# Optimization experiments

Hardware: AMD Instinct MI355X
Metric: run time of the kernel (lower is better)

The kernel has to match this reference:

```python
import jax, jax.numpy as jnp
import numpy as np

# Norse-style LIF constants (LIFParameters defaults, method='super', alpha=100)
DT = 0.001
TAU_SYN_INV = 200.0
TAU_MEM_INV = 100.0
V_TH = 1.0
V_LEAK = 0.0
V_RESET = 0.0
ALPHA = 100.0

@jax.custom_vjp
def heaviside(x):
    return (x > 0).astype(x.dtype)

def _heaviside_fwd(x):
    return heaviside(x), x

def _heaviside_bwd(x, g):
    # SuperSpike surrogate: 1 / (alpha*|x| + 1)^2
    return (g / (ALPHA * jnp.abs(x) + 1.0) ** 2,)

heaviside.defvjp(_heaviside_fwd, _heaviside_bwd)

def lif_step(v, i, inp_cur):
    # explicit-Euler LIF: membrane decays toward leak driven by synaptic current,
    # synaptic current decays, spikes reset membrane, input arrives as current jump
    v_dec = v + DT * TAU_MEM_INV * ((V_LEAK - v) + i)
    i_dec = i * (1.0 - DT * TAU_SYN_INV)
    z = heaviside(v_dec - V_TH)
    v_new = (1.0 - z) * v_dec + z * V_RESET
    i_new = i_dec + inp_cur
    return z, v_new, i_new

def li_step(v, i, inp_cur):
    # leaky integrator (non-spiking readout)
    v_new = v + DT * TAU_MEM_INV * ((V_LEAK - v) + i)
    i_new = i * (1.0 - DT * TAU_SYN_INV) + inp_cur
    return v_new, i_new


def setup_inputs() -> dict:
    key = jax.random.key(0)
    k1, k2, k3 = jax.random.split(key, 3)
    T, B = 64, 128
    FS2, H1, HC, OC, OUT = 4096, 2048, 2, 4, 10
    spl1, spl2 = FS2 // HC, H1 // OC
    x = jax.random.uniform(k1, (T, B, FS2), dtype=jnp.float32)
    w_hidden = jax.random.normal(k2, (HC, spl1, H1), dtype=jnp.float32) / np.sqrt(spl1)
    w_out = jax.random.normal(k3, (OC, spl2, OUT), dtype=jnp.float32) / np.sqrt(spl2)
    return {"x": x, "w_hidden": w_hidden, "w_out": w_out}


def reference(x, w_hidden, w_out):
    T, B, FS2 = x.shape
    HC, SPL1, H1 = w_hidden.shape
    OC, SPL2, OUT = w_out.shape
    f32 = x.dtype

    def step(carry, x_t):
        vdh, idh, vsh, ish, vdo, ido, vso, iso = carry
        # split input across hidden dendritic channels: [HC, B, SPL1]
        zc = x_t.reshape(B, HC, SPL1).transpose(1, 0, 2)
        cur_h = jnp.einsum('cbi,cio->cbo', zc, w_hidden)      # [HC, B, H1]
        s_d, vdh, idh = lif_step(vdh, idh, cur_h)             # dendritic spikes
        z_s, vsh, ish = lif_step(vsh, ish, s_d.sum(0))        # somatic spikes [B, H1]
        # split hidden spikes across output dendritic channels: [OC, B, SPL2]
        zo = z_s.reshape(B, OC, SPL2).transpose(1, 0, 2)
        cur_o = jnp.einsum('cbi,cio->cbo', zo, w_out)         # [OC, B, OUT]
        s_o, vdo, ido = lif_step(vdo, ido, cur_o)
        vso, iso = li_step(vso, iso, s_o.sum(0))              # readout voltage [B, OUT]
        return (vdh, idh, vsh, ish, vdo, ido, vso, iso), vso

    z = jnp.zeros
    carry0 = (z((HC, B, H1), f32), z((HC, B, H1), f32),
              z((B, H1), f32), z((B, H1), f32),
              z((OC, B, OUT), f32), z((OC, B, OUT), f32),
              z((B, OUT), f32), z((B, OUT), f32))
    _, voltages = jax.lax.scan(step, carry0, x)
    return voltages  # [T, B, 10]
```

## Files before the change

### kernel.cpp

```cpp
#include <hip/hip_runtime.h>

#define B 128
#define HC 2
#define H1 2048
#define FS2 4096
#define NK 2048
#define OC 4
#define SPL2 512
#define NOUT 10
#define T 64
#define HBH (HC*B*H1)

typedef __attribute__((ext_vector_type(8))) short bf16x8;
typedef __attribute__((ext_vector_type(4))) float f32x4;

__device__ __forceinline__ unsigned short f2bf(float f) {
  unsigned u = __float_as_uint(f);
  u += 0x7fff + ((u >> 16) & 1);
  return (unsigned short)(u >> 16);
}
__device__ __forceinline__ float bf2f(unsigned short s) {
  return __uint_as_float(((unsigned)s) << 16);
}

__device__ __forceinline__ void gload16(const void* g, void* l) {
  __builtin_amdgcn_global_load_lds(
      (const __attribute__((address_space(1))) unsigned int*)g,
      (__attribute__((address_space(3))) unsigned int*)l, 16, 0, 0);
}

__global__ __launch_bounds__(256) void init_state(float* __restrict__ p, int n) {
  int i = blockIdx.x * 256 + threadIdx.x;
  if (i < n) p[i] = 0.f;
}

__global__ __launch_bounds__(256) void conv_w(
    const float* __restrict__ w, unsigned short* __restrict__ wth,
    unsigned short* __restrict__ wtl) {
  __shared__ float s[64][65];
  const int c = blockIdx.z;
  const int n0 = blockIdx.x * 64, k0 = blockIdx.y * 64;
  const int tid = threadIdx.x;
  const int r = tid >> 4, c4 = (tid & 15) * 4;
#pragma unroll
  for (int q = 0; q < 4; ++q) {
    int kr = r + q * 16;
    float4 v = *(const float4*)(w + ((size_t)c * NK + k0 + kr) * H1 + n0 + c4);
    s[kr][c4 + 0] = v.x; s[kr][c4 + 1] = v.y;
    s[kr][c4 + 2] = v.z; s[kr][c4 + 3] = v.w;
  }
  __syncthreads();
#pragma unroll
  for (int q = 0; q < 4; ++q) {
    int nr = r + q * 16;
    float a0 = s[c4 + 0][nr], a1 = s[c4 + 1][nr];
    float a2 = s[c4 + 2][nr], a3 = s[c4 + 3][nr];
    ushort4 h, lo;
    h.x = f2bf(a0); h.y = f2bf(a1); h.z = f2bf(a2); h.w = f2bf(a3);
    lo.x = f2bf(a0 - bf2f(h.x)); lo.y = f2bf(a1 - bf2f(h.y));
    lo.z = f2bf(a2 - bf2f(h.z)); lo.w = f2bf(a3 - bf2f(h.w));
    size_t off = ((size_t)c * H1 + n0 + nr) * NK + k0 + c4;
    *(ushort4*)(wth + off) = h;
    *(ushort4*)(wtl + off) = lo;
  }
}

__global__ __launch_bounds__(512, 2) void gemm_split(
    const float* __restrict__ xA,
    const unsigned short* __restrict__ wth, const unsigned short* __restrict__ wtl,
    float* __restrict__ cur, int Mc, int nMblk) {
  const int bid = blockIdx.x;
  int c, nb, mb;
  if ((nMblk & 3) == 0) {
    const int xcd = bid & 7;
    const int slot = bid >> 3;
    c = xcd & 1;
    const int q = xcd >> 1;
    const int mq = nMblk >> 2;
    nb = slot & 7;
    mb = q * mq + (slot >> 3);
  } else {
    mb = bid % nMblk;
    int rest = bid / nMblk;
    nb = rest & 7;
    c = rest >> 3;
  }
  const int bm = mb * 256, bn = nb * 256;

  __shared__ unsigned short lds[65536];
  const int tid = threadIdx.x;

  unsigned dstOff[2]; size_t srcAf[2], srcB[2];
#pragma unroll
  for (int q = 0; q < 2; ++q) {
    int idx = q * 512 + tid;
    int row = idx >> 2, ps = idx & 3;
    int ks = (ps - (row >> 1)) & 3;
    int ar = bm + row; if (ar > Mc - 1) ar = Mc - 1;
    srcAf[q] = (size_t)ar * FS2 + (size_t)c * NK + ks * 8;
    srcB[q] = (size_t)c * NK * H1 + (size_t)(bn + row) * NK + ks * 8;
    dstOff[q] = idx * 8;
  }

  const int l = tid & 63, w = tid >> 6;
  const int wr = w >> 2, wc = w & 3;
  const int lrow = l & 15, lks = l >> 4;
  unsigned aoff[8], boff[4];
#pragma unroll
  for (int m = 0; m < 8; ++m) {
    int row = wr * 128 + m * 16 + lrow;
    int ps = (lks + (row >> 1)) & 3;
    aoff[m] = row * 32 + ps * 8;
  }
#pragma unroll
  for (int n = 0; n < 4; ++n) {
    int rn = wc * 64 + n * 16 + lrow;
    int ps = (lks + (rn >> 1)) & 3;
    boff[n] = rn * 32 + ps * 8;
  }

  f32x4 acc[8][4];
#pragma unroll
  for (int m = 0; m < 8; ++m)
#pragma unroll
    for (int n = 0; n < 4; ++n) acc[m][n] = (f32x4){0.f, 0.f, 0.f, 0.f};

  float4 fa[2][2];

#define LOAD_A(k0)                                                     \
  do {                                                                 \
    fa[0][0] = *(const float4*)(xA + srcAf[0] + (k0));                 \
    fa[0][1] = *(const float4*)(xA + srcAf[0] + (k0) + 4);             \
    fa[1][0] = *(const float4*)(xA + srcAf[1] + (k0));                 \
    fa[1][1] = *(const float4*)(xA + srcAf[1] + (k0) + 4);             \
  } while (0)
#define STAGE_BH(bufbase, k0)                                          \
  do {                                                                 \
    gload16(wth + srcB[0] + (k0), &lds[(bufbase) + 16384 + dstOff[0]]);\
    gload16(wth + srcB[1] + (k0), &lds[(bufbase) + 16384 + dstOff[1]]);\
  } while (0)
#define STAGE_BL(bufbase, k0)                                          \
  do {                                                                 \
    gload16(wtl + srcB[0] + (k0), &lds[(bufbase) + 24576 + dstOff[0]]);\
    gload16(wtl + srcB[1] + (k0), &lds[(bufbase) + 24576 + dstOff[1]]);\
  } while (0)
#define CVT_WRITE(bufbase)                                             \
  do {                                                                 \
    _Pragma("unroll")                                                  \
    for (int q = 0; q < 2; ++q) {                                      \
      union { unsigned short s[8]; bf16x8 v; } hi, lo;                 \
      const float* fp = (const float*)&fa[q][0];                       \
      _Pragma("unroll")                                                \
      for (int j = 0; j < 8; ++j) {                                    \
        unsigned short h = f2bf(fp[j]);                                \
        hi.s[j] = h;                                                   \
        lo.s[j] = (unsigned short)(__float_as_uint(fp[j] - bf2f(h)) >> 16); \
      }                                                                \
      *(bf16x8*)&lds[(bufbase) + dstOff[q]] = hi.v;                    \
      *(bf16x8*)&lds[(bufbase) + 8192 + dstOff[q]] = lo.v;             \
    }                                                                  \
  } while (0)

  const int NT = NK / 32;
  LOAD_A(0);
  STAGE_BH(0, 0);
  STAGE_BL(0, 0);
  asm volatile("s_waitcnt vmcnt(2)" ::: "memory");
  CVT_WRITE(0);

  for (int t = 0; t < NT; ++t) {
    const unsigned cb   = (unsigned)(t & 1) * 32768;
    const unsigned nbuf = (unsigned)((t + 1) & 1) * 32768;
    const int pf = (t + 1 < NT);
    const int kn = (t + 1) * 32;

    asm volatile("s_waitcnt vmcnt(2) lgkmcnt(0)\ns_barrier" ::: "memory");
    if (pf) { LOAD_A(kn); STAGE_BH(nbuf, kn); }
    bf16x8 bh[4], ah[8];
#pragma unroll
    for (int n = 0; n < 4; ++n) bh[n] = *(const bf16x8*)&lds[cb + 16384 + boff[n]];
#pragma unroll
    for (int m = 0; m < 8; ++m) ah[m] = *(const bf16x8*)&lds[cb + aoff[m]];
    asm volatile("s_waitcnt lgkmcnt(0)" ::: "memory");
    __builtin_amdgcn_sched_barrier(0);
    __builtin_amdgcn_s_setprio(1);
#pragma unroll
    for (int m = 0; m < 8; ++m)
#pragma unroll
      for (int n = 0; n < 4; ++n)
        acc[m][n] = __builtin_amdgcn_mfma_f32_16x16x32_bf16(ah[m], bh[n], acc[m][n], 0, 0, 0);
    __builtin_amdgcn_s_setprio(0);

    if (pf) asm volatile("s_waitcnt vmcnt(6)\ns_barrier" ::: "memory");
    else    asm volatile("s_waitcnt vmcnt(0)\ns_barrier" ::: "memory");
    if (pf) STAGE_BL(nbuf, kn);
    bf16x8 bl[4];
#pragma unroll
    for (int n = 0; n < 4; ++n) bl[n] = *(const bf16x8*)&lds[cb + 24576 + boff[n]];
    asm volatile("s_waitcnt lgkmcnt(0)" ::: "memory");
    __builtin_amdgcn_sched_barrier(0);
    __builtin_amdgcn_s_setprio(1);
#pragma unroll
    for (int m = 0; m < 8; ++m)
#pragma unroll
      for (int n = 0; n < 4; ++n)
        acc[m][n] = __builtin_amdgcn_mfma_f32_16x16x32_bf16(ah[m], bl[n], acc[m][n], 0, 0, 0);
    __builtin_amdgcn_s_setprio(0);

    bf16x8 al[8];
#pragma unroll
    for (int m = 0; m < 8; ++m) al[m] = *(const bf16x8*)&lds[cb + 8192 + aoff[m]];
    asm volatile("s_waitcnt lgkmcnt(0)" ::: "memory");
    __builtin_amdgcn_sched_barrier(0);
    __builtin_amdgcn_s_setprio(1);
#pragma unroll
    for (int m = 0; m < 8; ++m)
#pragma unroll
      for (int n = 0; n < 4; ++n)
        acc[m][n] = __builtin_amdgcn_mfma_f32_16x16x32_bf16(al[m], bh[n], acc[m][n], 0, 0, 0);
    __builtin_amdgcn_s_setprio(0);
    if (pf) {
      asm volatile("s_waitcnt vmcnt(2)" ::: "memory");
      CVT_WRITE(nbuf);
    }
  }
#undef LOAD_A
#undef STAGE_BH
#undef STAGE_BL
#undef CVT_WRITE

  float* Cc = cur + (size_t)c * Mc * H1;
#pragma unroll
  for (int m = 0; m < 8; ++m) {
    int grow = bm + wr * 128 + m * 16 + (l >> 4) * 4;
    if (grow < Mc) {
#pragma unroll
      for (int n = 0; n < 4; ++n) {
        int gcol = bn + wc * 64 + n * 16 + (l & 15);
        float* Cp = Cc + (size_t)grow * H1 + gcol;
        Cp[0]      = acc[m][n][0];
        Cp[H1]     = acc[m][n][1];
        Cp[2 * H1] = acc[m][n][2];
        Cp[3 * H1] = acc[m][n][3];
      }
    }
  }
}

__global__ __launch_bounds__(256) void seq_chunk(
    const float* __restrict__ cur, const float* __restrict__ wout,
    float* __restrict__ vdh, float* __restrict__ idh,
    float* __restrict__ vsh, float* __restrict__ ish,
    float* __restrict__ vdo, float* __restrict__ ido,
    float* __restrict__ sp_g, int t0, int tc, int Mc) {
  const int b = blockIdx.x >> 2;
  const int oc = blockIdx.x & 3;
  const int tid = threadIdx.x;
  __shared__ float wols[SPL2 * NOUT];
  __shared__ float zls[SPL2];
  __shared__ float cols[16];

#pragma unroll
  for (int q = 0; q < 5; ++q) {
    int i4 = q * 256 + tid;
    ((float4*)wols)[i4] = ((const float4*)(wout + (size_t)oc * SPL2 * NOUT))[i4];
  }
  const int hb = oc * SPL2;
  float vdl[HC][2], idl[HC][2], vsl[2], isl[2];
#pragma unroll
  for (int c = 0; c < HC; ++c)
#pragma unroll
    for (int u = 0; u < 2; ++u) {
      size_t o = ((size_t)c * B + b) * H1 + hb + tid + u * 256;
      vdl[c][u] = vdh[o]; idl[c][u] = idh[o];
    }
#pragma unroll
  for (int u = 0; u < 2; ++u) {
    size_t o = (size_t)b * H1 + hb + tid + u * 256;
    vsl[u] = vsh[o]; isl[u] = ish[o];
  }
  float vo = 0.f, io = 0.f;
  if (tid < NOUT) {
    vo = vdo[(oc * B + b) * NOUT + tid];
    io = ido[(oc * B + b) * NOUT + tid];
  }
  float pc[HC][2];
#pragma unroll
  for (int c = 0; c < HC; ++c)
#pragma unroll
    for (int u = 0; u < 2; ++u)
      pc[c][u] = cur[((size_t)c * Mc + b) * H1 + hb + tid + u * 256];

  for (int tl = 0; tl < tc; ++tl) {
#pragma unroll
    for (int u = 0; u < 2; ++u) {
      float zsum = 0.f;
#pragma unroll
      for (int c = 0; c < HC; ++c) {
        float v = vdl[c][u], i = idl[c][u];
        float vdec = v + 0.1f * (i - v);
        float idec = 0.8f * i;
        bool z = (vdec - 1.0f) > 0.f;
        vdl[c][u] = z ? 0.f : vdec;
        idl[c][u] = idec + pc[c][u];
        zsum += z ? 1.f : 0.f;
      }
      float v = vsl[u], i = isl[u];
      float vdec = v + 0.1f * (i - v);
      float idec = 0.8f * i;
      bool z = (vdec - 1.0f) > 0.f;
      vsl[u] = z ? 0.f : vdec;
      isl[u] = idec + zsum;
      zls[tid + u * 256] = z ? 1.f : 0.f;
    }
    if (tl + 1 < tc) {
#pragma unroll
      for (int c = 0; c < HC; ++c)
#pragma unroll
        for (int u = 0; u < 2; ++u)
          pc[c][u] = cur[((size_t)c * Mc + (tl + 1) * B + b) * H1 + hb + tid + u * 256];
    }
    __syncthreads();
    {
      const int g = tid >> 4, li = tid & 15;
      if (g < NOUT) {
        float s = 0.f;
#pragma unroll
        for (int j = 0; j < 32; ++j) {
          int i2 = li + 16 * j;
          s += zls[i2] * wols[i2 * NOUT + g];
        }
        s += __shfl_xor(s, 1); s += __shfl_xor(s, 2);
        s += __shfl_xor(s, 4); s += __shfl_xor(s, 8);
        if (li == 0) cols[g] = s;
      }
    }
    __syncthreads();
    if (tid < NOUT) {
      float vdec = vo + 0.1f * (io - vo);
      float idec = 0.8f * io;
      bool z = (vdec - 1.0f) > 0.f;
      vo = z ? 0.f : vdec;
      io = idec + cols[tid];
      sp_g[((size_t)(t0 + tl) * B + b) * (OC * NOUT) + oc * NOUT + tid] = z ? 1.f : 0.f;
    }
  }

#pragma unroll
  for (int c = 0; c < HC; ++c)
#pragma unroll
    for (int u = 0; u < 2; ++u) {
      size_t o = ((size_t)c * B + b) * H1 + hb + tid + u * 256;
      vdh[o] = vdl[c][u]; idh[o] = idl[c][u];
    }
#pragma unroll
  for (int u = 0; u < 2; ++u) {
    size_t o = (size_t)b * H1 + hb + tid + u * 256;
    vsh[o] = vsl[u]; ish[o] = isl[u];
  }
  if (tid < NOUT) {
    vdo[(oc * B + b) * NOUT + tid] = vo;
    ido[(oc * B + b) * NOUT + tid] = io;
  }
}

__global__ __launch_bounds__(256) void integrate_out(
    const float* __restrict__ sp_g, float* __restrict__ out) {
  int i = blockIdx.x * 256 + threadIdx.x;
  if (i >= B * NOUT) return;
  int b = i / NOUT, o = i % NOUT;
  float vr = 0.f, ir = 0.f;
  for (int t = 0; t < T; ++t) {
    const float* p = sp_g + ((size_t)(t * B + b) * OC) * NOUT + o;
    float ssum = ((p[0] + p[NOUT]) + p[2 * NOUT]) + p[3 * NOUT];
    float vn = vr + 0.1f * (ir - vr);
    ir = 0.8f * ir + ssum;
    vr = vn;
    out[(size_t)(t * B + b) * NOUT + o] = vn;
  }
}

extern "C" void kernel_launch(void* const* d_in, const int* in_sizes, int n_in,
                              void* d_out, int out_size, void* d_ws, size_t ws_size,
                              hipStream_t stream) {
  const float* x  = (const float*)d_in[0];
  const float* wh = (const float*)d_in[1];
  const float* wo = (const float*)d_in[2];
  float* out = (float*)d_out;
  char* ws = (char*)d_ws;

  unsigned short* wth = (unsigned short*)ws;
  unsigned short* wtl = wth + (size_t)HC * NK * H1;
  float* st  = (float*)(wtl + (size_t)HC * NK * H1);
  float* vdh = st;
  float* idh = vdh + HBH;
  float* vsh = idh + HBH;
  float* ish = vsh + (size_t)B * H1;
  float* vdo = ish + (size_t)B * H1;
  float* ido = vdo + OC * B * NOUT;
  float* sp_g = ido + OC * B * NOUT;
  float* dyn = sp_g + (size_t)T * B * OC * NOUT;
  const int NSTATE = (int)(sp_g - st);

  size_t fixed_bytes = (size_t)((char*)dyn - ws);
  size_t avail = (ws_size > fixed_bytes + 256) ? ws_size - fixed_bytes - 256 : 0;
  const size_t per_t = (size_t)HC * B * H1 * 4;
  int Tc = (int)(avail / per_t);
  if (Tc > T) Tc = T;
  if (Tc >= 8) Tc &= ~7;
  else if (Tc >= 2) Tc &= ~1;
  if (Tc < 1) Tc = 1;

  float* cur = dyn;

  init_state<<<(NSTATE + 255) / 256, 256, 0, stream>>>(st, NSTATE);
  conv_w<<<dim3(H1 / 64, NK / 64, HC), 256, 0, stream>>>(wh, wth, wtl);

  for (int t0 = 0; t0 < T; t0 += Tc) {
    int tc = (T - t0 < Tc) ? (T - t0) : Tc;
    int Mc = tc * B;
    int nMblk = (Mc + 255) / 256;
    gemm_split<<<HC * 8 * nMblk, 512, 0, stream>>>(
        x + (size_t)t0 * B * FS2, wth, wtl, cur, Mc, nMblk);
    seq_chunk<<<B * OC, 256, 0, stream>>>(cur, wo, vdh, idh, vsh, ish,
                                          vdo, ido, sp_g, t0, tc, Mc);
  }
  integrate_out<<<(B * NOUT + 255) / 256, 256, 0, stream>>>(sp_g, out);
}
```

Before: 434.2 us.

## Prefetch A operand two tiles ahead using double register banks

The fp32 A-tile global loads now run two K-tiles ahead, held in two alternating register banks (faA/faB), and the main loop is unrolled by two to swap banks. This gives the x loads a full extra tile of MFMA work to hide global latency before the bf16 hi/lo split and LDS write. The cost is more VGPRs for the second bank and retuned vmcnt wait counts, which risks lower occupancy or wrong waits if the counts are off.

```diff
diff --git a/kernel.cpp b/kernel.cpp
--- a/kernel.cpp
+++ b/kernel.cpp
@@ -125,14 +125,14 @@
 #pragma unroll
     for (int n = 0; n < 4; ++n) acc[m][n] = (f32x4){0.f, 0.f, 0.f, 0.f};
 
-  float4 fa[2][2];
-
-#define LOAD_A(k0)                                                     \
+  float4 faA[2][2], faB[2][2];
+
+#define LOAD_A(bank, k0)                                               \
   do {                                                                 \
-    fa[0][0] = *(const float4*)(xA + srcAf[0] + (k0));                 \
-    fa[0][1] = *(const float4*)(xA + srcAf[0] + (k0) + 4);             \
-    fa[1][0] = *(const float4*)(xA + srcAf[1] + (k0));                 \
-    fa[1][1] = *(const float4*)(xA + srcAf[1] + (k0) + 4);             \
+    bank[0][0] = *(const float4*)(xA + srcAf[0] + (k0));               \
+    bank[0][1] = *(const float4*)(xA + srcAf[0] + (k0) + 4);           \
+    bank[1][0] = *(const float4*)(xA + srcAf[1] + (k0));               \
+    bank[1][1] = *(const float4*)(xA + srcAf[1] + (k0) + 4);           \
   } while (0)
 #define STAGE_BH(bufbase, k0)                                          \
   do {                                                                 \
@@ -144,12 +144,12 @@
     gload16(wtl + srcB[0] + (k0), &lds[(bufbase) + 24576 + dstOff[0]]);\
     gload16(wtl + srcB[1] + (k0), &lds[(bufbase) + 24576 + dstOff[1]]);\
   } while (0)
-#define CVT_WRITE(bufbase)                                             \
+#define CVT_WRITE(bufbase, bank)                                       \
   do {                                                                 \
     _Pragma("unroll")                                                  \
     for (int q = 0; q < 2; ++q) {                                      \
       union { unsigned short s[8]; bf16x8 v; } hi, lo;                 \
-      const float* fp = (const float*)&fa[q][0];                       \
+      const float* fp = (const float*)&bank[q][0];                     \
       _Pragma("unroll")                                                \
       for (int j = 0; j < 8; ++j) {                                    \
         unsigned short h = f2bf(fp[j]);                                \
@@ -162,68 +162,82 @@
   } while (0)
 
   const int NT = NK / 32;
-  LOAD_A(0);
+
+  LOAD_A(faA, 0);
+  asm volatile("s_waitcnt vmcnt(0)" ::: "memory");
+  CVT_WRITE(0, faA);
   STAGE_BH(0, 0);
+  LOAD_A(faB, 32);
   STAGE_BL(0, 0);
-  asm volatile("s_waitcnt vmcnt(2)" ::: "memory");
-  CVT_WRITE(0);
-
-  for (int t = 0; t < NT; ++t) {
-    const unsigned cb   = (unsigned)(t & 1) * 32768;
-    const unsigned nbuf = (unsigned)((t + 1) & 1) * 32768;
-    const int pf = (t + 1 < NT);
-    const int kn = (t + 1) * 32;
-
-    asm volatile("s_waitcnt vmcnt(2) lgkmcnt(0)\ns_barrier" ::: "memory");
-    if (pf) { LOAD_A(kn); STAGE_BH(nbuf, kn); }
-    bf16x8 bh[4], ah[8];
-#pragma unroll
-    for (int n = 0; n < 4; ++n) bh[n] = *(const bf16x8*)&lds[cb + 16384 + boff[n]];
-#pragma unroll
-    for (int m = 0; m < 8; ++m) ah[m] = *(const bf16x8*)&lds[cb + aoff[m]];
-    asm volatile("s_waitcnt lgkmcnt(0)" ::: "memory");
-    __builtin_amdgcn_sched_barrier(0);
-    __builtin_amdgcn_s_setprio(1);
-#pragma unroll
-    for (int m = 0; m < 8; ++m)
-#pragma unroll
-      for (int n = 0; n < 4; ++n)
-        acc[m][n] = __builtin_amdgcn_mfma_f32_16x16x32_bf16(ah[m], bh[n], acc[m][n], 0, 0, 0);
-    __builtin_amdgcn_s_setprio(0);
-
-    if (pf) asm volatile("s_waitcnt vmcnt(6)\ns_barrier" ::: "memory");
-    else    asm volatile("s_waitcnt vmcnt(0)\ns_barrier" ::: "memory");
-    if (pf) STAGE_BL(nbuf, kn);
-    bf16x8 bl[4];
-#pragma unroll
-    for (int n = 0; n < 4; ++n) bl[n] = *(const bf16x8*)&lds[cb + 24576 + boff[n]];
-    asm volatile("s_waitcnt lgkmcnt(0)" ::: "memory");
-    __builtin_amdgcn_sched_barrier(0);
-    __builtin_amdgcn_s_setprio(1);
-#pragma unroll
-    for (int m = 0; m < 8; ++m)
-#pragma unroll
-      for (int n = 0; n < 4; ++n)
-        acc[m][n] = __builtin_amdgcn_mfma_f32_16x16x32_bf16(ah[m], bl[n], acc[m][n], 0, 0, 0);
-    __builtin_amdgcn_s_setprio(0);
-
-    bf16x8 al[8];
-#pragma unroll
-    for (int m = 0; m < 8; ++m) al[m] = *(const bf16x8*)&lds[cb + 8192 + aoff[m]];
-    asm volatile("s_waitcnt lgkmcnt(0)" ::: "memory");
-    __builtin_amdgcn_sched_barrier(0);
-    __builtin_amdgcn_s_setprio(1);
-#pragma unroll
-    for (int m = 0; m < 8; ++m)
-#pragma unroll
-      for (int n = 0; n < 4; ++n)
-        acc[m][n] = __builtin_amdgcn_mfma_f32_16x16x32_bf16(al[m], bh[n], acc[m][n], 0, 0, 0);
-    __builtin_amdgcn_s_setprio(0);
-    if (pf) {
-      asm volatile("s_waitcnt vmcnt(2)" ::: "memory");
-      CVT_WRITE(nbuf);
-    }
-  }
+
+#define TILE_BODY(T_, LOADBANK, CVTBANK)                                      \
+  do {                                                                        \
+    const int t_ = (T_);                                                      \
+    const unsigned cb   = (unsigned)(t_ & 1) * 32768;                         \
+    const unsigned nbuf = (unsigned)((t_ + 1) & 1) * 32768;                   \
+    const int kn = (t_ + 1) * 32;                                             \
+                                                                      \
+    if (t_ + 1 < NT)                                                          \
+      asm volatile("s_waitcnt vmcnt(6) lgkmcnt(0)\ns_barrier" ::: "memory");  \
+    else                                                                      \
+      asm volatile("s_waitcnt vmcnt(2) lgkmcnt(0)\ns_barrier" ::: "memory");  \
+    if (t_ + 1 < NT) STAGE_BH(nbuf, kn);                                      \
+    if (t_ + 2 < NT) LOAD_A(LOADBANK, (t_ + 2) * 32);                         \
+    bf16x8 bh[4], ah[8];                                                      \
+    _Pragma("unroll")                                                         \
+    for (int n = 0; n < 4; ++n) bh[n] = *(const bf16x8*)&lds[cb + 16384 + boff[n]]; \
+    _Pragma("unroll")                                                         \
+    for (int m = 0; m < 8; ++m) ah[m] = *(const bf16x8*)&lds[cb + aoff[m]];   \
+    asm volatile("s_waitcnt lgkmcnt(0)" ::: "memory");                        \
+    __builtin_amdgcn_sched_barrier(0);                                        \
+    __builtin_amdgcn_s_setprio(1);                                            \
+    _Pragma("unroll")                                                         \
+    for (int m = 0; m < 8; ++m)                                               \
+      _Pragma("unroll")                                                       \
+      for (int n = 0; n < 4; ++n)                                             \
+        acc[m][n] = __builtin_amdgcn_mfma_f32_16x16x32_bf16(ah[m], bh[n], acc[m][n], 0, 0, 0); \
+    __builtin_amdgcn_s_setprio(0);                                            \
+                                                                      \
+    if (t_ + 2 < NT)                                                          \
+      asm volatile("s_waitcnt vmcnt(6)\ns_barrier" ::: "memory");             \
+    else if (t_ + 1 < NT)                                                     \
+      asm volatile("s_waitcnt vmcnt(2)\ns_barrier" ::: "memory");             \
+    else                                                                      \
+      asm volatile("s_waitcnt vmcnt(0)\ns_barrier" ::: "memory");             \
+    if (t_ + 1 < NT) STAGE_BL(nbuf, kn);                                      \
+    bf16x8 bl[4];                                                             \
+    _Pragma("unroll")                                                         \
+    for (int n = 0; n < 4; ++n) bl[n] = *(const bf16x8*)&lds[cb + 24576 + boff[n]]; \
+    asm volatile("s_waitcnt lgkmcnt(0)" ::: "memory");                        \
+    __builtin_amdgcn_sched_barrier(0);                                        \
+    __builtin_amdgcn_s_setprio(1);                                            \
+    _Pragma("unroll")                                                         \
+    for (int m = 0; m < 8; ++m)                                               \
+      _Pragma("unroll")                                                       \
+      for (int n = 0; n < 4; ++n)                                             \
+        acc[m][n] = __builtin_amdgcn_mfma_f32_16x16x32_bf16(ah[m], bl[n], acc[m][n], 0, 0, 0); \
+    __builtin_amdgcn_s_setprio(0);                                            \
+                                                         \
+    bf16x8 al[8];                                                             \
+    _Pragma("unroll")                                                         \
+    for (int m = 0; m < 8; ++m) al[m] = *(const bf16x8*)&lds[cb + 8192 + aoff[m]]; \
+    asm volatile("s_waitcnt lgkmcnt(0)" ::: "memory");                        \
+    __builtin_amdgcn_sched_barrier(0);                                        \
+    __builtin_amdgcn_s_setprio(1);                                            \
+    _Pragma("unroll")                                                         \
+    for (int m = 0; m < 8; ++m)                                               \
+      _Pragma("unroll")                                                       \
+      for (int n = 0; n < 4; ++n)                                             \
+        acc[m][n] = __builtin_amdgcn_mfma_f32_16x16x32_bf16(al[m], bh[n], acc[m][n], 0, 0, 0); \
+    __builtin_amdgcn_s_setprio(0);                                            \
+    if (t_ + 1 < NT) CVT_WRITE(nbuf, CVTBANK);   \
+  } while (0)
+
+  for (int t = 0; t < NT; t += 2) {
+    TILE_BODY(t, faA, faB);
+    TILE_BODY(t + 1, faB, faA);
+  }
+#undef TILE_BODY
 #undef LOAD_A
 #undef STAGE_BH
 #undef STAGE_BL
```

New measurement: 694.4 us. 1.6x slower.
